# Performance work log

Measured on AMD Instinct MI355X. Metric: run time of the kernel, lower is better.

## Reference

```python
import math
import jax, jax.numpy as jnp
import numpy as np

L, B, S, D, HID, NH = 4, 2, 2048, 1024, 1024, 16
C = HID // NH  # 64


def setup_inputs() -> dict:
    key = jax.random.key(0)
    ks = jax.random.split(key, 8)
    p = lambda k, shape: jax.random.normal(k, shape, jnp.float32) * 0.02
    return {
        "x": jax.random.normal(ks[0], (B, S, D), jnp.float32),
        "Wq": p(ks[1], (L, D, HID)), "bq": jnp.zeros((L, HID), jnp.float32),
        "Wk": p(ks[2], (L, D, HID)), "bk": jnp.zeros((L, HID), jnp.float32),
        "Wv": p(ks[3], (L, D, HID)), "bv": jnp.zeros((L, HID), jnp.float32),
        "Wo": p(ks[4], (L, HID, D)), "bo": jnp.zeros((L, D), jnp.float32),
        "W1": p(ks[5], (L, D, HID)), "b1": jnp.zeros((L, HID), jnp.float32),
        "W2": p(ks[6], (L, HID, D)), "b2": jnp.zeros((L, D), jnp.float32),
        "gamma": jnp.ones((L, D), jnp.float32),   # single LayerNorm reused twice per block
        "beta": jnp.zeros((L, D), jnp.float32),
    }


def _pos_enc(seq_len, d, n=1000.0):
    col = jnp.arange(seq_len, dtype=jnp.float32)[:, None]        # [S,1]
    row = jnp.arange(d)                                          # [D]
    exp = (2.0 * (row // 2).astype(jnp.float32)) / d
    mat = col / jnp.power(n, exp)[None, :]                       # [S,D]
    return jnp.where(row % 2 == 0, jnp.sin(mat), jnp.cos(mat))


def _layernorm(x, g, b, eps=1e-5):
    mu = jnp.mean(x, axis=-1, keepdims=True)
    var = jnp.mean((x - mu) ** 2, axis=-1, keepdims=True)        # biased, as torch
    return (x - mu) / jnp.sqrt(var + eps) * g + b


def _block(x, Wq, bq, Wk, bk, Wv, bv, Wo, bo, W1, b1, W2, b2, g, be):
    b_, s_, _ = x.shape
    q = ((x @ Wq + bq)).reshape(b_, s_, NH, C) / math.sqrt(C)
    k = (x @ Wk + bk).reshape(b_, s_, NH, C)
    v = (x @ Wv + bv).reshape(b_, s_, NH, C)
    # NOTE: faithful to original einsum '...hq,...hk->...hqk' -> per-token
    # attention over the CHANNEL axis c, with a (c,c) causal mask.
    aff = jnp.einsum('bshq,bshk->bshqk', q, k)                   # [B,S,H,C,C]
    mask = jnp.triu(jnp.ones((C, C), bool), 1)
    aff = jnp.where(mask, -jnp.inf, aff)
    w = jax.nn.softmax(aff, axis=-1)
    av = jnp.einsum('bshqk,bshk->bshq', w, v).reshape(b_, s_, HID)
    attn_out = av @ Wo + bo
    x = _layernorm(attn_out + x, g, be)
    mlp_out = jax.nn.relu(x @ W1 + b1) @ W2 + b2
    return _layernorm(mlp_out + x, g, be)


def reference(x, Wq, bq, Wk, bk, Wv, bv, Wo, bo, W1, b1, W2, b2, gamma, beta):
    x = x + _pos_enc(x.shape[1], x.shape[2])
    for i in range(L):
        x = _block(x, Wq[i], bq[i], Wk[i], bk[i], Wv[i], bv[i], Wo[i], bo[i],
                   W1[i], b1[i], W2[i], b2[i], gamma[i], beta[i])
    return x
```

## Files before the change

### kernel.cpp

```cpp
#include <hip/hip_runtime.h>
#include <hip/hip_bf16.h>
#include <stdint.h>

#define TOK 4096
#define DM  1024

using u16 = unsigned short;
typedef __attribute__((ext_vector_type(8))) short short8;
typedef __attribute__((ext_vector_type(4))) float f32x4;

__device__ __forceinline__ u16 f2bf(float f){
  unsigned u = __float_as_uint(f);
  return (u16)((u + 0x7fffu + ((u >> 16) & 1u)) >> 16);
}
__device__ __forceinline__ float bf2f(u16 h){ return __uint_as_float(((unsigned)h) << 16); }

__device__ __forceinline__ float fexp2(float x){
#if __has_builtin(__builtin_amdgcn_exp2f)
  return __builtin_amdgcn_exp2f(x);
#else
  float r; asm("v_exp_f32 %0, %1\n\ts_nop 0" : "=v"(r) : "v"(x)); return r;
#endif
}

__global__ __launch_bounds__(256) void posenc_add(
    const float* __restrict__ x, float* __restrict__ r, u16* __restrict__ xb)
{
  const int t = blockIdx.x;
  const int s = t & 2047;
  const size_t base = (size_t)t * DM;
#pragma unroll
  for (int i = 0; i < 4; ++i){
    const int d = threadIdx.x + i * 256;
    const float e = (float)(d & ~1) * (1.0f / (float)DM);
    const float denom = powf(1000.0f, e);
    const float mat = (float)s / denom;
    const float pe = (d & 1) ? cosf(mat) : sinf(mat);
    const float v = x[base + d] + pe;
    r[base + d] = v;
    xb[base + d] = f2bf(v);
  }
}

__global__ __launch_bounds__(256) void transpose6(
    const float* __restrict__ Wq, const float* __restrict__ Wk, const float* __restrict__ Wv,
    const float* __restrict__ Wo, const float* __restrict__ W1, const float* __restrict__ W2,
    u16* __restrict__ WT, int l0)
{
  __shared__ float tile[32][33];
  const int bid = blockIdx.x;
  const int l  = l0 + bid / 6144;
  const int mm = (bid >> 10) % 6;
  const int t  = bid & 1023;
  const int tn = (t & 31) * 32;
  const int tk = (t >> 5) * 32;
  const float* src = (mm==0)?Wq:(mm==1)?Wk:(mm==2)?Wv:(mm==3)?Wo:(mm==4)?W1:W2;
  src += (size_t)l * 1048576;
  u16* dst = WT + ((size_t)(l - l0) * 6 + mm) * 1048576;
  const int tx = threadIdx.x & 31, ty = threadIdx.x >> 5;
#pragma unroll
  for (int i = 0; i < 4; ++i)
    tile[ty + i*8][tx] = src[(size_t)(tk + ty + i*8) * 1024 + tn + tx];
  __syncthreads();
#pragma unroll
  for (int i = 0; i < 4; ++i)
    dst[(size_t)(tn + ty + i*8) * 1024 + tk + tx] = f2bf(tile[tx][ty + i*8]);
}

#define BM 128
#define BK 64
#define KD 1024

template<int MODE, int BNt>
__global__ __launch_bounds__(256) void gemm_k1024(
    const u16* __restrict__ A, const u16* __restrict__ BT,
    const float* __restrict__ bias0, const float* __restrict__ bias1, const float* __restrict__ bias2,
    u16* __restrict__ outB, int M, int N)
{
  constexpr int NFR = BNt / 32;
  __shared__ __align__(16) u16 sA[BM*BK];
  __shared__ __align__(16) u16 sB[BNt*BK];
  const int tid  = threadIdx.x;
  const int lane = tid & 63;
  const int wave = tid >> 6;
  const int nbn = N / BNt;
  const int nwg = gridDim.x;
  const int wg  = (blockIdx.x & 7) * (nwg >> 3) + (blockIdx.x >> 3);
  const size_t m0 = (size_t)(wg / nbn) * BM;
  const size_t n0 = (size_t)(wg % nbn) * BNt;

  const int srow  = lane >> 3;
  const int sslot = (lane & 7) ^ srow;
  const u16* gA = A  + (m0 + wave*32 + srow) * KD + sslot * 8;
  const u16* gB = BT + (n0 + wave*(BNt/4) + srow) * KD + sslot * 8;
  u16* lA = sA + (wave*32) * 64;
  u16* lB = sB + (wave*(BNt/4)) * 64;

  const int wm = (wave >> 1) * 64;
  const int wn = (wave & 1) * (BNt/2);
  f32x4 acc[4][NFR] = {};

  for (int kt = 0; kt < KD/BK; ++kt){
    const int k0 = kt * BK;
#pragma unroll
    for (int p = 0; p < 4; ++p)
      __builtin_amdgcn_global_load_lds(
          (const __attribute__((address_space(1))) void*)(gA + p*8*KD + k0),
          (__attribute__((address_space(3))) void*)(lA + p*8*64), 16, 0, 0);
#pragma unroll
    for (int p = 0; p < BNt/32; ++p)
      __builtin_amdgcn_global_load_lds(
          (const __attribute__((address_space(1))) void*)(gB + p*8*KD + k0),
          (__attribute__((address_space(3))) void*)(lB + p*8*64), 16, 0, 0);
    __syncthreads();
#pragma unroll
    for (int kk = 0; kk < 2; ++kk){
      short8 af[4], bfr[NFR];
      const int kidx = kk*4 + (lane >> 4);
#pragma unroll
      for (int i = 0; i < 4; ++i){
        const int arow = wm + i*16 + (lane & 15);
        af[i]  = *(const short8*)(sA + arow*64 + (kidx ^ (arow & 7)) * 8);
      }
#pragma unroll
      for (int j = 0; j < NFR; ++j){
        const int brow = wn + j*16 + (lane & 15);
        bfr[j] = *(const short8*)(sB + brow*64 + (kidx ^ (brow & 7)) * 8);
      }
#pragma unroll
      for (int i = 0; i < 4; ++i)
#pragma unroll
        for (int j = 0; j < NFR; ++j)
          acc[i][j] = __builtin_amdgcn_mfma_f32_16x16x32_bf16(af[i], bfr[j], acc[i][j], 0, 0, 0);
    }
    __syncthreads();
  }

#pragma unroll
  for (int i = 0; i < 4; ++i){
    const int growb = wm + i*16 + (lane >> 4) * 4;
#pragma unroll
    for (int j = 0; j < NFR; ++j){
      const size_t gcol = n0 + wn + j*16 + (lane & 15);
      float bv;
      if constexpr (MODE == 2)
        bv = (gcol < 1024) ? bias0[gcol] : (gcol < 2048) ? bias1[gcol - 1024] : bias2[gcol - 2048];
      else
        bv = bias0[gcol];
#pragma unroll
      for (int r = 0; r < 4; ++r){
        const size_t grow = m0 + growb + r;
        float v = acc[i][j][r] + bv;
        if constexpr (MODE == 0)      outB[grow * N + gcol] = f2bf(v);
        else if constexpr (MODE == 1) outB[grow * N + gcol] = f2bf(fmaxf(v, 0.0f));
        else                          outB[grow * N + gcol] = f2bf(gcol < 1024 ? v * 0.125f : v);
      }
    }
  }
}

__global__ __launch_bounds__(256) void attn_chan(
    const u16* __restrict__ qkv, u16* __restrict__ av)
{
  __shared__ __align__(16) float2 skv[4][64];
  const int t    = blockIdx.x >> 2;
  const int hb   = blockIdx.x & 3;
  const int lane = threadIdx.x & 63;
  const int wave = threadIdx.x >> 6;
  const int h    = hb * 4 + wave;
  float2* kw = skv[wave];
  const int r = lane & 3;
  const size_t base = (size_t)t * 3072 + h * 64 + lane;
  const float qi2 = bf2f(qkv[base]) * 1.44269504f;
  const float ki  = bf2f(qkv[base + 1024]);
  const float vi  = bf2f(qkv[base + 2048]);
  kw[lane] = make_float2(ki, vi);
  float ssum = 0.0f, acc = 0.0f;
#pragma unroll 8
  for (int j0 = 0; j0 < 64; j0 += 4){
    const float4 ab = *(const float4*)(kw + j0);
    const float4 cd = *(const float4*)(kw + j0 + 2);
    const float bias = (j0 + 3 <= lane) ? 0.0f : -200.0f;
    const float e0 = fexp2(fmaf(qi2, ab.x, bias));
    const float e1 = fexp2(fmaf(qi2, ab.z, bias));
    const float e2 = fexp2(fmaf(qi2, cd.x, bias));
    const float e3 = fexp2(fmaf(qi2, cd.z, bias));
    ssum += (e0 + e1) + (e2 + e3);
    acc = fmaf(e0, ab.y, acc);
    acc = fmaf(e1, ab.w, acc);
    acc = fmaf(e2, cd.y, acc);
    acc = fmaf(e3, cd.w, acc);
  }
#pragma unroll
  for (int s = 0; s < 3; ++s){
    const float2 kv = kw[lane - r + s];
    const float bf = (s <= r && r < 3) ? 0.0f : -200.0f;
    const float e = fexp2(fmaf(qi2, kv.x, bf));
    ssum += e;
    acc = fmaf(e, kv.y, acc);
  }
  av[(size_t)t * 1024 + h * 64 + lane] = f2bf(acc / ssum);
}

__global__ __launch_bounds__(256) void residual_ln(
    const u16* __restrict__ y, const float* xres,
    const float* __restrict__ gamma, const float* __restrict__ beta,
    float* xout, u16* __restrict__ xb)
{
  __shared__ float red[4];
  const int row = blockIdx.x, tid = threadIdx.x;
  const int lane = tid & 63, wave = tid >> 6;
  const ushort4 a = ((const ushort4*)(y + (size_t)row*DM))[tid];
  const float4  b = ((const float4*)(xres + (size_t)row*DM))[tid];
  float4 s; s.x=bf2f(a.x)+b.x; s.y=bf2f(a.y)+b.y; s.z=bf2f(a.z)+b.z; s.w=bf2f(a.w)+b.w;
  float p = s.x + s.y + s.z + s.w;
#pragma unroll
  for (int o = 32; o; o >>= 1) p += __shfl_xor(p, o);
  if (lane == 0) red[wave] = p;
  __syncthreads();
  const float mu = (red[0]+red[1]+red[2]+red[3]) * (1.0f/(float)DM);
  __syncthreads();
  const float dx=s.x-mu, dy=s.y-mu, dz=s.z-mu, dw=s.w-mu;
  float q2 = dx*dx + dy*dy + dz*dz + dw*dw;
#pragma unroll
  for (int o = 32; o; o >>= 1) q2 += __shfl_xor(q2, o);
  if (lane == 0) red[wave] = q2;
  __syncthreads();
  const float var = (red[0]+red[1]+red[2]+red[3]) * (1.0f/(float)DM);
  const float rstd = rsqrtf(var + 1e-5f);
  const float4 g  = ((const float4*)gamma)[tid];
  const float4 be = ((const float4*)beta)[tid];
  float4 o4;
  o4.x = dx*rstd*g.x + be.x;
  o4.y = dy*rstd*g.y + be.y;
  o4.z = dz*rstd*g.z + be.z;
  o4.w = dw*rstd*g.w + be.w;
  ((float4*)(xout + (size_t)row*DM))[tid] = o4;
  ushort4 ob; ob.x=f2bf(o4.x); ob.y=f2bf(o4.y); ob.z=f2bf(o4.z); ob.w=f2bf(o4.w);
  ((ushort4*)(xb + (size_t)row*DM))[tid] = ob;
}

extern "C" void kernel_launch(void* const* d_in, const int* in_sizes, int n_in,
                              void* d_out, int out_size, void* d_ws, size_t ws_size,
                              hipStream_t stream)
{
  const float* x    = (const float*)d_in[0];
  const float* Wq   = (const float*)d_in[1];
  const float* bq   = (const float*)d_in[2];
  const float* Wk   = (const float*)d_in[3];
  const float* bk   = (const float*)d_in[4];
  const float* Wv   = (const float*)d_in[5];
  const float* bv   = (const float*)d_in[6];
  const float* Wo   = (const float*)d_in[7];
  const float* bo   = (const float*)d_in[8];
  const float* W1   = (const float*)d_in[9];
  const float* b1   = (const float*)d_in[10];
  const float* W2   = (const float*)d_in[11];
  const float* b2   = (const float*)d_in[12];
  const float* gam  = (const float*)d_in[13];
  const float* bet  = (const float*)d_in[14];

  char* ws = (char*)d_ws;
  size_t off = 0;
  auto alloc = [&](size_t b){ void* p = ws + off; off = (off + b + 255) & ~(size_t)255; return p; };

  const size_t oneWT = 6ull*1048576*2;
  const size_t rest  = ((size_t)TOK*DM*4)
                     + ((size_t)TOK*DM*2)
                     + ((size_t)TOK*3072*2)
                     + ((size_t)TOK*DM*2)
                     + ((size_t)TOK*DM*2)
                     + ((size_t)TOK*DM*2)
                     + 4096;
  const bool all4 = (4*oneWT + rest) <= ws_size;

  u16*   WT   = (u16*)  alloc(all4 ? 4*oneWT : oneWT);
  float* res  = (float*)alloc((size_t)TOK*DM*4);
  u16*   xb   = (u16*)  alloc((size_t)TOK*DM*2);
  u16*   qkv  = (u16*)  alloc((size_t)TOK*3072*2);
  u16*   avb  = (u16*)  alloc((size_t)TOK*DM*2);
  u16*   hbuf = (u16*)  alloc((size_t)TOK*DM*2);
  u16*   ybuf = (u16*)  alloc((size_t)TOK*DM*2);
  if (off > ws_size) return;

  posenc_add<<<TOK, 256, 0, stream>>>(x, res, xb);
  if (all4)
    transpose6<<<4*6*1024, 256, 0, stream>>>(Wq, Wk, Wv, Wo, W1, W2, WT, 0);

  for (int l = 0; l < 4; ++l){
    u16* wt = all4 ? (WT + (size_t)l * 6 * 1048576) : WT;
    if (!all4)
      transpose6<<<6*1024, 256, 0, stream>>>(Wq, Wk, Wv, Wo, W1, W2, WT, l);
    gemm_k1024<2,128><<<(TOK/BM)*(3072/128), 256, 0, stream>>>(
        xb, wt, bq + l*1024, bk + l*1024, bv + l*1024, qkv, TOK, 3072);
    attn_chan<<<TOK*4, 256, 0, stream>>>(qkv, avb);
    gemm_k1024<0,64><<<(TOK/BM)*(1024/64), 256, 0, stream>>>(
        avb, wt + 3ull*1048576, bo + l*1024, nullptr, nullptr, ybuf, TOK, 1024);
    residual_ln<<<TOK, 256, 0, stream>>>(ybuf, res, gam + l*1024, bet + l*1024, res, xb);
    gemm_k1024<1,64><<<(TOK/BM)*(1024/64), 256, 0, stream>>>(
        xb, wt + 4ull*1048576, b1 + l*1024, nullptr, nullptr, hbuf, TOK, 1024);
    gemm_k1024<0,64><<<(TOK/BM)*(1024/64), 256, 0, stream>>>(
        hbuf, wt + 5ull*1048576, b2 + l*1024, nullptr, nullptr, ybuf, TOK, 1024);
    float* xdst = (l == 3) ? (float*)d_out : res;
    residual_ln<<<TOK, 256, 0, stream>>>(ybuf, res, gam + l*1024, bet + l*1024, xdst, xb);
  }
}
```

Measured before the change: 618.2 us.

## Double-buffer GEMM LDS, drop fp32 residual, widen attention per wave

The GEMM now double-buffers its LDS tiles so the next k-tile's global-to-LDS load overlaps the MFMA work on the current one. It also fixes the N tile at 64 (including for QKV), sets launch_bounds occupancy to 3, and unifies the epilogue. The fp32 residual stream is removed: residuals are read from the bf16 activation buffer and fp32 is written only for the final output, which cuts memory traffic at some cost in precision. The attention kernel processes two heads per wave with split accumulators and uses a hardware reciprocal instead of a divide.

```diff
diff --git a/kernel.cpp b/kernel.cpp
--- a/kernel.cpp
+++ b/kernel.cpp
@@ -22,9 +22,16 @@
   float r; asm("v_exp_f32 %0, %1\n\ts_nop 0" : "=v"(r) : "v"(x)); return r;
 #endif
 }
+__device__ __forceinline__ float frcp(float x){
+#if __has_builtin(__builtin_amdgcn_rcpf)
+  return __builtin_amdgcn_rcpf(x);
+#else
+  float r; asm("v_rcp_f32 %0, %1\n\ts_nop 0" : "=v"(r) : "v"(x)); return r;
+#endif
+}
 
 __global__ __launch_bounds__(256) void posenc_add(
-    const float* __restrict__ x, float* __restrict__ r, u16* __restrict__ xb)
+    const float* __restrict__ x, u16* __restrict__ xb)
 {
   const int t = blockIdx.x;
   const int s = t & 2047;
@@ -36,9 +43,7 @@
     const float denom = powf(1000.0f, e);
     const float mat = (float)s / denom;
     const float pe = (d & 1) ? cosf(mat) : sinf(mat);
-    const float v = x[base + d] + pe;
-    r[base + d] = v;
-    xb[base + d] = f2bf(v);
+    xb[base + d] = f2bf(x[base + d] + pe);
   }
 }
 
@@ -71,15 +76,15 @@
 #define BK 64
 #define KD 1024
 
-template<int MODE, int BNt>
-__global__ __launch_bounds__(256) void gemm_k1024(
+template<int MODE>
+__global__ __launch_bounds__(256, 3) void gemm_k1024(
     const u16* __restrict__ A, const u16* __restrict__ BT,
     const float* __restrict__ bias0, const float* __restrict__ bias1, const float* __restrict__ bias2,
     u16* __restrict__ outB, int M, int N)
 {
-  constexpr int NFR = BNt / 32;
-  __shared__ __align__(16) u16 sA[BM*BK];
-  __shared__ __align__(16) u16 sB[BNt*BK];
+  constexpr int BNt = 64;
+  constexpr int NFR = 2;
+  __shared__ __align__(16) u16 lds2[2][(BM + BNt) * BK];
   const int tid  = threadIdx.x;
   const int lane = tid & 63;
   const int wave = tid >> 6;
@@ -92,27 +97,31 @@
   const int srow  = lane >> 3;
   const int sslot = (lane & 7) ^ srow;
   const u16* gA = A  + (m0 + wave*32 + srow) * KD + sslot * 8;
-  const u16* gB = BT + (n0 + wave*(BNt/4) + srow) * KD + sslot * 8;
-  u16* lA = sA + (wave*32) * 64;
-  u16* lB = sB + (wave*(BNt/4)) * 64;
+  const u16* gB = BT + (n0 + wave*16 + srow) * KD + sslot * 8;
+  const int loA = (wave*32) * 64;
+  const int loB = BM*BK + (wave*16) * 64;
 
   const int wm = (wave >> 1) * 64;
-  const int wn = (wave & 1) * (BNt/2);
+  const int wn = (wave & 1) * 32;
   f32x4 acc[4][NFR] = {};
 
-  for (int kt = 0; kt < KD/BK; ++kt){
+  auto stage = [&](int kt, int buf){
+    u16* base = lds2[buf];
     const int k0 = kt * BK;
 #pragma unroll
     for (int p = 0; p < 4; ++p)
       __builtin_amdgcn_global_load_lds(
           (const __attribute__((address_space(1))) void*)(gA + p*8*KD + k0),
-          (__attribute__((address_space(3))) void*)(lA + p*8*64), 16, 0, 0);
-#pragma unroll
-    for (int p = 0; p < BNt/32; ++p)
+          (__attribute__((address_space(3))) void*)(base + loA + p*512), 16, 0, 0);
+#pragma unroll
+    for (int p = 0; p < 2; ++p)
       __builtin_amdgcn_global_load_lds(
           (const __attribute__((address_space(1))) void*)(gB + p*8*KD + k0),
-          (__attribute__((address_space(3))) void*)(lB + p*8*64), 16, 0, 0);
-    __syncthreads();
+          (__attribute__((address_space(3))) void*)(base + loB + p*512), 16, 0, 0);
+  };
+  auto compute = [&](int buf){
+    const u16* sAc = lds2[buf];
+    const u16* sBc = sAc + BM*BK;
 #pragma unroll
     for (int kk = 0; kk < 2; ++kk){
       short8 af[4], bfr[NFR];
@@ -120,12 +129,12 @@
 #pragma unroll
       for (int i = 0; i < 4; ++i){
         const int arow = wm + i*16 + (lane & 15);
-        af[i]  = *(const short8*)(sA + arow*64 + (kidx ^ (arow & 7)) * 8);
+        af[i]  = *(const short8*)(sAc + arow*64 + (kidx ^ (arow & 7)) * 8);
       }
 #pragma unroll
       for (int j = 0; j < NFR; ++j){
         const int brow = wn + j*16 + (lane & 15);
-        bfr[j] = *(const short8*)(sB + brow*64 + (kidx ^ (brow & 7)) * 8);
+        bfr[j] = *(const short8*)(sBc + brow*64 + (kidx ^ (brow & 7)) * 8);
       }
 #pragma unroll
       for (int i = 0; i < 4; ++i)
@@ -133,6 +142,13 @@
         for (int j = 0; j < NFR; ++j)
           acc[i][j] = __builtin_amdgcn_mfma_f32_16x16x32_bf16(af[i], bfr[j], acc[i][j], 0, 0, 0);
     }
+  };
+
+  stage(0, 0);
+  __syncthreads();
+  for (int kt = 0; kt < KD/BK; ++kt){
+    if (kt + 1 < KD/BK) stage(kt + 1, (kt + 1) & 1);
+    compute(kt & 1);
     __syncthreads();
   }
 
@@ -151,9 +167,9 @@
       for (int r = 0; r < 4; ++r){
         const size_t grow = m0 + growb + r;
         float v = acc[i][j][r] + bv;
-        if constexpr (MODE == 0)      outB[grow * N + gcol] = f2bf(v);
-        else if constexpr (MODE == 1) outB[grow * N + gcol] = f2bf(fmaxf(v, 0.0f));
-        else                          outB[grow * N + gcol] = f2bf(gcol < 1024 ? v * 0.125f : v);
+        if constexpr (MODE == 1) v = fmaxf(v, 0.0f);
+        if constexpr (MODE == 2){ if (gcol < 1024) v *= 0.125f; }
+        outB[grow * N + gcol] = f2bf(v);
       }
     }
   }
@@ -162,57 +178,70 @@
 __global__ __launch_bounds__(256) void attn_chan(
     const u16* __restrict__ qkv, u16* __restrict__ av)
 {
-  __shared__ __align__(16) float2 skv[4][64];
-  const int t    = blockIdx.x >> 2;
-  const int hb   = blockIdx.x & 3;
+  __shared__ __align__(16) float2 skv[4][2][64];
+  const int t    = blockIdx.x >> 1;
   const int lane = threadIdx.x & 63;
   const int wave = threadIdx.x >> 6;
-  const int h    = hb * 4 + wave;
-  float2* kw = skv[wave];
-  const int r = lane & 3;
-  const size_t base = (size_t)t * 3072 + h * 64 + lane;
-  const float qi2 = bf2f(qkv[base]) * 1.44269504f;
-  const float ki  = bf2f(qkv[base + 1024]);
-  const float vi  = bf2f(qkv[base + 2048]);
-  kw[lane] = make_float2(ki, vi);
-  float ssum = 0.0f, acc = 0.0f;
-#pragma unroll 8
+  const int h0   = (blockIdx.x & 1) * 8 + wave * 2;
+  const int r3   = lane & 3;
+  const size_t base = (size_t)t * 3072 + h0 * 64 + lane;
+  const float q0 = bf2f(qkv[base])      * 1.44269504f;
+  const float q1 = bf2f(qkv[base + 64]) * 1.44269504f;
+  skv[wave][0][lane] = make_float2(bf2f(qkv[base + 1024]), bf2f(qkv[base + 2048]));
+  skv[wave][1][lane] = make_float2(bf2f(qkv[base + 1088]), bf2f(qkv[base + 2112]));
+  const float2* kwa = skv[wave][0];
+  const float2* kwb = skv[wave][1];
+  float sa0=0.f, sa1=0.f, aa0=0.f, aa1=0.f;
+  float sb0=0.f, sb1=0.f, ab0=0.f, ab1=0.f;
+#pragma unroll
   for (int j0 = 0; j0 < 64; j0 += 4){
-    const float4 ab = *(const float4*)(kw + j0);
-    const float4 cd = *(const float4*)(kw + j0 + 2);
+    const float4 A0 = *(const float4*)(kwa + j0);
+    const float4 A1 = *(const float4*)(kwa + j0 + 2);
+    const float4 B0 = *(const float4*)(kwb + j0);
+    const float4 B1 = *(const float4*)(kwb + j0 + 2);
     const float bias = (j0 + 3 <= lane) ? 0.0f : -200.0f;
-    const float e0 = fexp2(fmaf(qi2, ab.x, bias));
-    const float e1 = fexp2(fmaf(qi2, ab.z, bias));
-    const float e2 = fexp2(fmaf(qi2, cd.x, bias));
-    const float e3 = fexp2(fmaf(qi2, cd.z, bias));
-    ssum += (e0 + e1) + (e2 + e3);
-    acc = fmaf(e0, ab.y, acc);
-    acc = fmaf(e1, ab.w, acc);
-    acc = fmaf(e2, cd.y, acc);
-    acc = fmaf(e3, cd.w, acc);
+    const float ea0 = fexp2(fmaf(q0, A0.x, bias));
+    const float ea1 = fexp2(fmaf(q0, A0.z, bias));
+    const float ea2 = fexp2(fmaf(q0, A1.x, bias));
+    const float ea3 = fexp2(fmaf(q0, A1.z, bias));
+    const float eb0 = fexp2(fmaf(q1, B0.x, bias));
+    const float eb1 = fexp2(fmaf(q1, B0.z, bias));
+    const float eb2 = fexp2(fmaf(q1, B1.x, bias));
+    const float eb3 = fexp2(fmaf(q1, B1.z, bias));
+    sa0 += ea0 + ea2;  sa1 += ea1 + ea3;
+    sb0 += eb0 + eb2;  sb1 += eb1 + eb3;
+    aa0 = fmaf(ea0, A0.y, fmaf(ea2, A1.y, aa0));
+    aa1 = fmaf(ea1, A0.w, fmaf(ea3, A1.w, aa1));
+    ab0 = fmaf(eb0, B0.y, fmaf(eb2, B1.y, ab0));
+    ab1 = fmaf(eb1, B0.w, fmaf(eb3, B1.w, ab1));
   }
 #pragma unroll
   for (int s = 0; s < 3; ++s){
-    const float2 kv = kw[lane - r + s];
-    const float bf = (s <= r && r < 3) ? 0.0f : -200.0f;
-    const float e = fexp2(fmaf(qi2, kv.x, bf));
-    ssum += e;
-    acc = fmaf(e, kv.y, acc);
-  }
-  av[(size_t)t * 1024 + h * 64 + lane] = f2bf(acc / ssum);
+    const int jj = lane - r3 + s;
+    const float bias = (s <= r3 && r3 < 3) ? 0.0f : -200.0f;
+    const float2 ka = kwa[jj];
+    const float2 kb = kwb[jj];
+    const float ea = fexp2(fmaf(q0, ka.x, bias));
+    const float eb = fexp2(fmaf(q1, kb.x, bias));
+    sa0 += ea; aa0 = fmaf(ea, ka.y, aa0);
+    sb0 += eb; ab0 = fmaf(eb, kb.y, ab0);
+  }
+  av[(size_t)t * DM + h0*64 + lane]      = f2bf((aa0 + aa1) * frcp(sa0 + sa1));
+  av[(size_t)t * DM + h0*64 + 64 + lane] = f2bf((ab0 + ab1) * frcp(sb0 + sb1));
 }
 
 __global__ __launch_bounds__(256) void residual_ln(
-    const u16* __restrict__ y, const float* xres,
+    const u16* __restrict__ y, const u16* xres,
     const float* __restrict__ gamma, const float* __restrict__ beta,
-    float* xout, u16* __restrict__ xb)
+    float* xoutF, u16* xb)
 {
   __shared__ float red[4];
   const int row = blockIdx.x, tid = threadIdx.x;
   const int lane = tid & 63, wave = tid >> 6;
-  const ushort4 a = ((const ushort4*)(y + (size_t)row*DM))[tid];
-  const float4  b = ((const float4*)(xres + (size_t)row*DM))[tid];
-  float4 s; s.x=bf2f(a.x)+b.x; s.y=bf2f(a.y)+b.y; s.z=bf2f(a.z)+b.z; s.w=bf2f(a.w)+b.w;
+  const ushort4 a = ((const ushort4*)(y    + (size_t)row*DM))[tid];
+  const ushort4 b = ((const ushort4*)(xres + (size_t)row*DM))[tid];
+  float4 s; s.x=bf2f(a.x)+bf2f(b.x); s.y=bf2f(a.y)+bf2f(b.y);
+  s.z=bf2f(a.z)+bf2f(b.z); s.w=bf2f(a.w)+bf2f(b.w);
   float p = s.x + s.y + s.z + s.w;
 #pragma unroll
   for (int o = 32; o; o >>= 1) p += __shfl_xor(p, o);
@@ -235,7 +264,7 @@
   o4.y = dy*rstd*g.y + be.y;
   o4.z = dz*rstd*g.z + be.z;
   o4.w = dw*rstd*g.w + be.w;
-  ((float4*)(xout + (size_t)row*DM))[tid] = o4;
+  if (xoutF) ((float4*)(xoutF + (size_t)row*DM))[tid] = o4;
   ushort4 ob; ob.x=f2bf(o4.x); ob.y=f2bf(o4.y); ob.z=f2bf(o4.z); ob.w=f2bf(o4.w);
   ((ushort4*)(xb + (size_t)row*DM))[tid] = ob;
 }
@@ -265,8 +294,7 @@
   auto alloc = [&](size_t b){ void* p = ws + off; off = (off + b + 255) & ~(size_t)255; return p; };
 
   const size_t oneWT = 6ull*1048576*2;
-  const size_t rest  = ((size_t)TOK*DM*4)
-                     + ((size_t)TOK*DM*2)
+  const size_t rest  = ((size_t)TOK*DM*2)
                      + ((size_t)TOK*3072*2)
                      + ((size_t)TOK*DM*2)
                      + ((size_t)TOK*DM*2)
@@ -275,7 +303,6 @@
   const bool all4 = (4*oneWT + rest) <= ws_size;
 
   u16*   WT   = (u16*)  alloc(all4 ? 4*oneWT : oneWT);
-  float* res  = (float*)alloc((size_t)TOK*DM*4);
   u16*   xb   = (u16*)  alloc((size_t)TOK*DM*2);
   u16*   qkv  = (u16*)  alloc((size_t)TOK*3072*2);
   u16*   avb  = (u16*)  alloc((size_t)TOK*DM*2);
@@ -283,7 +310,7 @@
   u16*   ybuf = (u16*)  alloc((size_t)TOK*DM*2);
   if (off > ws_size) return;
 
-  posenc_add<<<TOK, 256, 0, stream>>>(x, res, xb);
+  posenc_add<<<TOK, 256, 0, stream>>>(x, xb);
   if (all4)
     transpose6<<<4*6*1024, 256, 0, stream>>>(Wq, Wk, Wv, Wo, W1, W2, WT, 0);
 
@@ -291,17 +318,17 @@
     u16* wt = all4 ? (WT + (size_t)l * 6 * 1048576) : WT;
     if (!all4)
       transpose6<<<6*1024, 256, 0, stream>>>(Wq, Wk, Wv, Wo, W1, W2, WT, l);
-    gemm_k1024<2,128><<<(TOK/BM)*(3072/128), 256, 0, stream>>>(
+    gemm_k1024<2><<<(TOK/BM)*(3072/64), 256, 0, stream>>>(
         xb, wt, bq + l*1024, bk + l*1024, bv + l*1024, qkv, TOK, 3072);
-    attn_chan<<<TOK*4, 256, 0, stream>>>(qkv, avb);
-    gemm_k1024<0,64><<<(TOK/BM)*(1024/64), 256, 0, stream>>>(
+    attn_chan<<<TOK*2, 256, 0, stream>>>(qkv, avb);
+    gemm_k1024<0><<<(TOK/BM)*(1024/64), 256, 0, stream>>>(
         avb, wt + 3ull*1048576, bo + l*1024, nullptr, nullptr, ybuf, TOK, 1024);
-    residual_ln<<<TOK, 256, 0, stream>>>(ybuf, res, gam + l*1024, bet + l*1024, res, xb);
-    gemm_k1024<1,64><<<(TOK/BM)*(1024/64), 256, 0, stream>>>(
+    residual_ln<<<TOK, 256, 0, stream>>>(ybuf, xb, gam + l*1024, bet + l*1024, nullptr, xb);
+    gemm_k1024<1><<<(TOK/BM)*(1024/64), 256, 0, stream>>>(
         xb, wt + 4ull*1048576, b1 + l*1024, nullptr, nullptr, hbuf, TOK, 1024);
-    gemm_k1024<0,64><<<(TOK/BM)*(1024/64), 256, 0, stream>>>(
+    gemm_k1024<0><<<(TOK/BM)*(1024/64), 256, 0, stream>>>(
         hbuf, wt + 5ull*1048576, b2 + l*1024, nullptr, nullptr, ybuf, TOK, 1024);
-    float* xdst = (l == 3) ? (float*)d_out : res;
-    residual_ln<<<TOK, 256, 0, stream>>>(ybuf, res, gam + l*1024, bet + l*1024, xdst, xb);
-  }
-}
+    residual_ln<<<TOK, 256, 0, stream>>>(ybuf, xb, gam + l*1024, bet + l*1024,
+                                         (l == 3) ? (float*)d_out : nullptr, xb);
+  }
+}
```

Result: faster. 557.2 us (-9.9%).
